# Kernel tuning notes

Measured on AMD Instinct MI355X. Metric: run time of the kernel, lower is better.

Reference implementation:

```python
import jax, jax.numpy as jnp
import numpy as np

N = 50000   # num_entities
F = 300     # node feature dim
D = 128     # embedding_dim
H = 4       # heads
C = D // H  # per-head out channels (32)
E = 640000  # num edges
R = 200     # num_relations
L = 2       # num_layers
NEG_SLOPE = 0.2  # PyG GATv2Conv default


def setup_inputs() -> dict:
    key = jax.random.key(0)
    ks = jax.random.split(key, 14)
    s = 0.1
    return {
        "entity": jnp.arange(N, dtype=jnp.int32),
        "edge_index": jax.random.randint(ks[0], (2, E), 0, N, dtype=jnp.int32),
        "edge_type": jax.random.randint(ks[1], (E,), 0, R, dtype=jnp.int32),
        # learned parameters
        "node_features": jax.random.normal(ks[2], (N, F), jnp.float32) * s,   # entity_embedding table
        "rel_emb": jax.random.normal(ks[3], (R, D), jnp.float32) * s,          # relation_embedding
        "proj_w": jax.random.normal(ks[4], (F, D), jnp.float32) * s,           # project Linear
        "proj_b": jnp.zeros((D,), jnp.float32),
        # per-layer GATv2Conv params, stacked over L layers
        "w_l": jax.random.normal(ks[5], (L, D, H * C), jnp.float32) * s,       # lin_l weight
        "b_l": jnp.zeros((L, H * C), jnp.float32),
        "w_r": jax.random.normal(ks[6], (L, D, H * C), jnp.float32) * s,       # lin_r weight
        "b_r": jnp.zeros((L, H * C), jnp.float32),
        "w_e": jax.random.normal(ks[7], (L, D, H * C), jnp.float32) * s,       # lin_edge weight (no bias)
        "att": jax.random.normal(ks[8], (L, H, C), jnp.float32) * s,           # attention vector a
        "bias": jnp.zeros((L, H * C), jnp.float32),                             # output bias
    }


def _gatv2_layer(x, src, dst, edge_attr, w_l, b_l, w_r, b_r, w_e, att, bias):
    # x: [N, D], edge_attr: [E, D]
    x_l = (x @ w_l + b_l).reshape(N, H, C)
    x_r = (x @ w_r + b_r).reshape(N, H, C)
    e = (edge_attr @ w_e).reshape(E, H, C)
    # per-edge message (gather src/dst + edge), GATv2: leaky_relu BEFORE attention dot
    m = jax.nn.leaky_relu(x_l[src] + x_r[dst] + e, NEG_SLOPE)   # [E, H, C]
    logits = jnp.einsum('ehc,hc->eh', m, att)                    # [E, H]
    # segment softmax over edges grouped by destination node
    lmax = jax.ops.segment_max(logits, dst, num_segments=N)      # [N, H]
    ex = jnp.exp(logits - lmax[dst])                             # [E, H]
    denom = jax.ops.segment_sum(ex, dst, num_segments=N)         # [N, H]
    alpha = ex / denom[dst]                                      # [E, H]
    # scatter-aggregate messages x_l[src] weighted by alpha
    out = jax.ops.segment_sum(x_l[src] * alpha[:, :, None], dst, num_segments=N)  # [N, H, C]
    return out.reshape(N, H * C) + bias


def reference(entity, edge_index, edge_type, node_features, rel_emb,
              proj_w, proj_b, w_l, b_l, w_r, b_r, w_e, att, bias):
    x = node_features[entity]            # embedding lookup
    x = x @ proj_w + proj_b              # project to D
    edge_attr = rel_emb[edge_type]       # [E, D] (weights=False -> no edge_weight scaling)
    src, dst = edge_index[0], edge_index[1]
    for i in range(L):
        x = _gatv2_layer(x, src, dst, edge_attr,
                         w_l[i], b_l[i], w_r[i], b_r[i], w_e[i], att[i], bias[i])
        if i != L - 1:
            x = jax.nn.elu(x)            # dropout inactive (eval mode)
    return x
```

## Files before the change

kernel.cpp:

```cpp
#include <hip/hip_runtime.h>

#define NN 50000
#define FF 300
#define DD 128
#define HH 4
#define CC 32
#define EE 640000
#define RR 200
#define LL 2
#define SB ((NN + 255) / 256)
#define PK 320
#define WCONV (2 * 128 * 128)
#define WTOT (2 * 128 * PK + WCONV)
#define HB2 (EE / 1024)
#define WB2 (WCONV / 1024)
#define FB2 80
#define RB2 100
#define NCH (NN * (PK / 8))
#define CVB3 ((NCH + 1023) / 1024)
#define SCB (EE / 1024)

typedef unsigned short u16;
typedef unsigned int u32;
typedef unsigned long long u64;
typedef _Float16 h2   __attribute__((ext_vector_type(2)));
typedef _Float16 half8 __attribute__((ext_vector_type(8)));
typedef __attribute__((ext_vector_type(4))) float floatx4;
typedef u32 u32x4 __attribute__((ext_vector_type(4)));
typedef u32 u32x2 __attribute__((ext_vector_type(2)));

__device__ __forceinline__ u16 f2h(float f) {
    union { _Float16 h; u16 u; } v; v.h = (_Float16)f; return v.u;
}
__device__ __forceinline__ h2 u2h2(u32 p) {
    union { u32 u; h2 h; } v; v.u = p; return v.h;
}
__device__ __forceinline__ h2 hmax2(h2 a, h2 b) {
#if __has_builtin(__builtin_elementwise_max)
    return __builtin_elementwise_max(a, b);
#else
    h2 r; r.x = a.x > b.x ? a.x : b.x; r.y = a.y > b.y ? a.y : b.y; return r;
#endif
}
__device__ __forceinline__ float hdot2(h2 a, h2 b, float c) {
#if __has_builtin(__builtin_amdgcn_fdot2)
    return __builtin_amdgcn_fdot2(a, b, c, false);
#else
    return c + (float)a.x * (float)b.x + (float)a.y * (float)b.y;
#endif
}
__device__ __forceinline__ void glds16(const void* g, void* l) {
    using gp = const unsigned int __attribute__((address_space(1)))*;
    using lp = unsigned int __attribute__((address_space(3)))*;
    __builtin_amdgcn_global_load_lds((gp)(u64)g, (lp)(u64)l, 16, 0, 0);
}

__device__ __forceinline__ int block_excl_scan(int v, int* lds4, int* total) {
    int lane = threadIdx.x & 63, wid = threadIdx.x >> 6;
    int x = v;
    #pragma unroll
    for (int off = 1; off < 64; off <<= 1) {
        int y = __shfl_up(x, off, 64);
        if (lane >= off) x += y;
    }
    if (lane == 63) lds4[wid] = x;
    __syncthreads();
    int add = 0;
    #pragma unroll
    for (int w = 0; w < 4; w++) add += (w < wid) ? lds4[w] : 0;
    *total = lds4[0] + lds4[1] + lds4[2] + lds4[3];
    return x + add - v;
}

__global__ __launch_bounds__(256)
void prep_kernel(const int* __restrict__ ei, int* __restrict__ counts,
                 const float* __restrict__ proj_w, const float* __restrict__ w_l,
                 const float* __restrict__ w_r, u16* __restrict__ wt,
                 const float* __restrict__ rel_emb, const float* __restrict__ w_e,
                 u16* __restrict__ erel, const float* __restrict__ proj_b,
                 const float* __restrict__ b_l, const float* __restrict__ b_r,
                 float* __restrict__ fbias, const int* __restrict__ entity,
                 const float* __restrict__ nf, u16* __restrict__ xh)
{
    __shared__ float sm[8 * DD];
    int b = blockIdx.x, tid = threadIdx.x;
    if (b < HB2) {
        #pragma unroll
        for (int j = 0; j < 4; j++)
            atomicAdd(&counts[ei[EE + b * 1024 + j * 256 + tid]], 1);
    } else if (b < HB2 + WB2) {
        #pragma unroll
        for (int j = 0; j < 4; j++) {
            int i = (b - HB2) * 1024 + j * 256 + tid;
            int seg = i >> 14;
            int r = i & 16383;
            int n = r >> 7, k = r & 127;
            const float* src = (seg == 0 ? w_l : w_r) + (size_t)DD * DD;
            wt[2 * 128 * PK + i] = f2h(src[(size_t)k * DD + n]);
        }
    } else if (b < HB2 + WB2 + FB2) {
        int bb = b - HB2 - WB2;
        int lr = bb / 40, kg = bb % 40;
        int half = tid >> 7, d = tid & 127;
        int k0 = kg * 8 + half * 4;
        float* rv = sm + half * 4 * DD;
        #pragma unroll
        for (int kk = 0; kk < 4; kk++)
            rv[kk * DD + d] = (k0 + kk < FF) ? proj_w[(size_t)(k0 + kk) * DD + d] : 0.f;
        __syncthreads();
        const float* W = lr ? w_r : w_l;
        float acc[4] = {0.f, 0.f, 0.f, 0.f};
        #pragma unroll 8
        for (int j = 0; j < DD; j++) {
            float wv = W[(size_t)j * DD + d];
            #pragma unroll
            for (int kk = 0; kk < 4; kk++) acc[kk] += rv[kk * DD + j] * wv;
        }
        u16 o[4];
        #pragma unroll
        for (int kk = 0; kk < 4; kk++) o[kk] = f2h(acc[kk]);
        *(u32x2*)(wt + (size_t)lr * 128 * PK + (size_t)d * PK + k0) = *(u32x2*)o;
    } else if (b == HB2 + WB2 + FB2) {
        int half = tid >> 7, d = tid & 127;
        if (tid < DD) sm[tid] = proj_b[tid];
        __syncthreads();
        const float* W = half ? w_r : w_l;
        float acc = half ? b_r[d] : b_l[d];
        #pragma unroll 8
        for (int j = 0; j < DD; j++) acc += sm[j] * W[(size_t)j * DD + d];
        fbias[half * DD + d] = acc;
    } else if (b < HB2 + WB2 + FB2 + 1 + RB2) {
        int bb = b - (HB2 + WB2 + FB2 + 1);
        int l = bb / 50, rg = bb % 50;
        int half = tid >> 7, d = tid & 127;
        int r0 = rg * 4 + half * 2;
        float* rv = sm + half * 2 * DD;
        #pragma unroll
        for (int rr = 0; rr < 2; rr++)
            rv[rr * DD + d] = rel_emb[(size_t)(r0 + rr) * DD + d];
        __syncthreads();
        const float* W = w_e + (size_t)l * DD * DD;
        float acc[2] = {0.f, 0.f};
        #pragma unroll 8
        for (int j = 0; j < DD; j++) {
            float wv = W[(size_t)j * DD + d];
            #pragma unroll
            for (int rr = 0; rr < 2; rr++) acc[rr] += rv[rr * DD + j] * wv;
        }
        #pragma unroll
        for (int rr = 0; rr < 2; rr++)
            erel[(size_t)(l * RR + r0 + rr) * DD + d] = f2h(acc[rr]);
    } else {
        int base = (b - (HB2 + WB2 + FB2 + 1 + RB2)) * 1024 + tid;
        #pragma unroll
        for (int j = 0; j < 4; j++) {
            int ci = base + j * 256;
            if (ci < NCH) {
                int row = ci / (PK / 8);
                int col = (ci - row * (PK / 8)) * 8;
                int xrow = entity[row];
                const float* src = nf + (size_t)xrow * FF + col;
                u16 o[8];
                if (col + 8 <= FF) {
                    float4 f0 = *(const float4*)src;
                    float4 f1 = *(const float4*)(src + 4);
                    o[0] = f2h(f0.x); o[1] = f2h(f0.y); o[2] = f2h(f0.z); o[3] = f2h(f0.w);
                    o[4] = f2h(f1.x); o[5] = f2h(f1.y); o[6] = f2h(f1.z); o[7] = f2h(f1.w);
                } else {
                    #pragma unroll
                    for (int jj = 0; jj < 8; jj++)
                        o[jj] = (col + jj < FF) ? f2h(src[jj]) : (u16)0;
                }
                *(half8*)(xh + (size_t)row * PK + col) = *(half8*)o;
            }
        }
    }
}

template<int K>
__global__ __launch_bounds__(512)
void gemm_gll_kernel(const u16* __restrict__ A,
                     const u16* __restrict__ BT1, const float* __restrict__ bias1,
                     u16* __restrict__ C1,
                     const u16* __restrict__ BT2, const float* __restrict__ bias2,
                     u16* __restrict__ C2, int M)
{
    __shared__ u16 As[64 * 64];
    __shared__ u16 Bs[256 * 64];
    int tid  = threadIdx.x;
    int m0   = blockIdx.x * 64;
    int wave = tid >> 6, lane = tid & 63;
    int quad = lane >> 4, l16 = lane & 15;

    floatx4 acc[4][2];
    #pragma unroll
    for (int i = 0; i < 4; i++)
        #pragma unroll
        for (int j = 0; j < 2; j++) acc[i][j] = (floatx4){0.f, 0.f, 0.f, 0.f};

    int arl = wave * 8 + (lane >> 3);
    int arg = m0 + arl; if (arg >= M) arg = M - 1;
    const char* ap = (const char*)(A + (size_t)arg * K)
                   + (((lane & 7) << 4) ^ ((arl & 7) << 4));
    const char* bp[4];
    #pragma unroll
    for (int c = 0; c < 4; c++) {
        int rowB = wave * 32 + c * 8 + (lane >> 3);
        const u16* base = (rowB < 128) ? BT1 : BT2;
        int br = rowB & 127;
        bp[c] = (const char*)(base + (size_t)br * K)
              + (((lane & 7) << 4) ^ ((br & 7) << 4));
    }
    char* AsW = (char*)As;
    char* BsW = (char*)Bs;
    const char* AsR = (const char*)As;
    const char* BsR = (const char*)Bs;
    int axor = (l16 & 7) << 4;

    for (int kk = 0; kk < K; kk += 64) {
        glds16(ap + kk * 2, AsW + wave * 1024);
        #pragma unroll
        for (int c = 0; c < 4; c++)
            glds16(bp[c] + kk * 2, BsW + (wave * 4 + c) * 1024);
        __syncthreads();
        #pragma unroll
        for (int s2 = 0; s2 < 2; s2++) {
            int cb = (s2 * 64 + quad * 16) ^ axor;
            half8 af[4], bf[2];
            #pragma unroll
            for (int i = 0; i < 4; i++)
                af[i] = *(const half8*)(AsR + (i * 16 + l16) * 128 + cb);
            #pragma unroll
            for (int j = 0; j < 2; j++)
                bf[j] = *(const half8*)(BsR + (wave * 32 + j * 16 + l16) * 128 + cb);
            #pragma unroll
            for (int i = 0; i < 4; i++) {
                acc[i][0] = __builtin_amdgcn_mfma_f32_16x16x32_f16(af[i], bf[0], acc[i][0], 0, 0, 0);
                acc[i][1] = __builtin_amdgcn_mfma_f32_16x16x32_f16(af[i], bf[1], acc[i][1], 0, 0, 0);
            }
        }
        __syncthreads();
    }

    u16* Cw = (wave < 4) ? C1 : C2;
    const float* bw = (wave < 4) ? bias1 : bias2;
    int cb0 = (wave & 3) * 32;
    #pragma unroll
    for (int i = 0; i < 4; i++) {
        #pragma unroll
        for (int rr = 0; rr < 4; rr++) {
            int row = m0 + i * 16 + quad * 4 + rr;
            if (row < M) {
                #pragma unroll
                for (int j = 0; j < 2; j++) {
                    int col = cb0 + j * 16 + l16;
                    Cw[(size_t)row * DD + col] = f2h(acc[i][j][rr] + bw[col]);
                }
            }
        }
    }
}

__global__ __launch_bounds__(256)
void scan_local_kernel(const int* __restrict__ counts, int* __restrict__ offsets,
                       int* __restrict__ bsum)
{
    __shared__ int lds4[4];
    int i = blockIdx.x * 256 + threadIdx.x;
    int v = (i < NN) ? counts[i] : 0;
    int total;
    int ex = block_excl_scan(v, lds4, &total);
    if (i < NN) offsets[i] = ex;
    if (threadIdx.x == 0) bsum[blockIdx.x] = total;
}

__global__ __launch_bounds__(256)
void scan_bsum_kernel(int* __restrict__ bsum)
{
    __shared__ int lds4[4];
    int t = threadIdx.x;
    int v = (t < SB) ? bsum[t] : 0;
    int total;
    int ex = block_excl_scan(v, lds4, &total);
    if (t < SB) bsum[t] = ex;
}

__global__ __launch_bounds__(256)
void scatter_kernel(const int* __restrict__ ei, const int* __restrict__ et,
                    const int* __restrict__ offsets, const int* __restrict__ bsum,
                    int* __restrict__ fill, u32* __restrict__ dstorder)
{
    #pragma unroll
    for (int j = 0; j < 4; j++) {
        int e = blockIdx.x * 1024 + j * 256 + threadIdx.x;
        int d = ei[EE + e];
        int pos = offsets[d] + bsum[d >> 8] + atomicAdd(&fill[d], 1);
        dstorder[pos] = (u32)ei[e] | ((u32)et[e] << 16);
    }
}

__global__ __launch_bounds__(256)
void node_kernel(const u32* __restrict__ dstorder, const int* __restrict__ offsets,
                 const int* __restrict__ bsum,
                 const u16* __restrict__ xl, const u16* __restrict__ xr,
                 const u16* __restrict__ erel, const float* __restrict__ att,
                 const float* __restrict__ bias,
                 u16* __restrict__ xnext, float* __restrict__ outp, int is_last)
{
    int tid  = threadIdx.x;
    int node = blockIdx.x * 4 + (tid >> 6);
    int lane = tid & 63;
    if (node >= NN) return;
    int g  = lane >> 4;
    int gl = lane & 15;
    int c0 = gl * 8;
    int beg = offsets[node] + bsum[node >> 8];
    int end = (node == NN - 1) ? EE : offsets[node + 1] + bsum[(node + 1) >> 8];

    h2 xrh[4], atth[4];
    {
        u32x4 xrv = *(const u32x4*)(xr + ((u32)node * DD + c0));
        #pragma unroll
        for (int q = 0; q < 4; q++) xrh[q] = u2h2(xrv[q]);
        #pragma unroll
        for (int q = 0; q < 4; q++) {
            float2 av = *(const float2*)&att[c0 + q * 2];
            atth[q] = (h2){(_Float16)av.x, (_Float16)av.y};
        }
    }
    const h2 c02 = (h2){(_Float16)0.2f, (_Float16)0.2f};

    float s = 0.f;
    h2 a2[4];
    #pragma unroll
    for (int q = 0; q < 4; q++) a2[q] = (h2){(_Float16)0.f, (_Float16)0.f};

    for (int base = beg; base < end; base += 4) {
        int es = base + g;
        bool valid = es < end;
        u32 st = valid ? dstorder[es] : 0;
        u32 xoff = (st & 0xffffu) * DD + (u32)c0;
        u32 eoff = (st >> 16) * DD + (u32)c0;
        u32x4 xv = *(const u32x4*)(xl + xoff);
        u32x4 ev = *(const u32x4*)(erel + eoff);
        h2 xh[4];
        float p = 0.f;
        #pragma unroll
        for (int q = 0; q < 4; q++) {
            xh[q] = u2h2(xv[q]);
            h2 m = (xh[q] + xrh[q]) + u2h2(ev[q]);
            m = hmax2(m, m * c02);
            p = hdot2(m, atth[q], p);
        }
        p += __shfl_xor(p, 1, 64);
        p += __shfl_xor(p, 2, 64);
        float w = valid ? __expf(fminf(p, 60.f)) : 0.f;
        s += w;
        h2 wh = (h2){(_Float16)w, (_Float16)w};
        #pragma unroll
        for (int q = 0; q < 4; q++) a2[q] += wh * xh[q];
    }

    float a[8];
    #pragma unroll
    for (int q = 0; q < 4; q++) { a[q*2] = (float)a2[q].x; a[q*2+1] = (float)a2[q].y; }
    #pragma unroll
    for (int j = 0; j < 8; j++) {
        a[j] += __shfl_xor(a[j], 16, 64);
        a[j] += __shfl_xor(a[j], 32, 64);
    }
    s += __shfl_xor(s, 16, 64);
    s += __shfl_xor(s, 32, 64);

    if (lane < 16) {
        float rh = 1.f / fmaxf(s, 1e-30f);
        float4 b0 = *(const float4*)&bias[c0];
        float4 b1 = *(const float4*)&bias[c0 + 4];
        float bv[8] = {b0.x, b0.y, b0.z, b0.w, b1.x, b1.y, b1.z, b1.w};
        float v[8];
        #pragma unroll
        for (int j = 0; j < 8; j++) v[j] = a[j] * rh + bv[j];
        if (is_last) {
            float4* op = (float4*)(outp + ((u32)node * DD + c0));
            op[0] = make_float4(v[0], v[1], v[2], v[3]);
            op[1] = make_float4(v[4], v[5], v[6], v[7]);
        } else {
            u16 pk[8];
            #pragma unroll
            for (int j = 0; j < 8; j++) {
                float w2 = v[j] > 0.f ? v[j] : __expf(v[j]) - 1.f;
                pk[j] = f2h(w2);
            }
            *(half8*)(xnext + ((u32)node * DD + c0)) = *(half8*)pk;
        }
    }
}

extern "C" void kernel_launch(void* const* d_in, const int* in_sizes, int n_in,
                              void* d_out, int out_size, void* d_ws, size_t ws_size,
                              hipStream_t stream)
{
    const int*   entity        = (const int*)d_in[0];
    const int*   edge_index    = (const int*)d_in[1];
    const int*   edge_type     = (const int*)d_in[2];
    const float* node_features = (const float*)d_in[3];
    const float* rel_emb       = (const float*)d_in[4];
    const float* proj_w        = (const float*)d_in[5];
    const float* proj_b        = (const float*)d_in[6];
    const float* w_l           = (const float*)d_in[7];
    const float* b_l           = (const float*)d_in[8];
    const float* w_r           = (const float*)d_in[9];
    const float* b_r           = (const float*)d_in[10];
    const float* w_e           = (const float*)d_in[11];
    const float* att           = (const float*)d_in[12];
    const float* bias          = (const float*)d_in[13];

    u16*   xb      = (u16*)d_ws;
    u16*   xl      = xb + (size_t)NN * DD;
    u16*   xr      = xl + (size_t)NN * DD;
    u16*   erel    = xr + (size_t)NN * DD;
    u16*   wt      = erel + (size_t)LL * RR * DD;
    u32*   dstorder= (u32*)(wt + WTOT);
    int*   counts  = (int*)(dstorder + (size_t)EE);
    int*   fill    = counts + NN;
    int*   offsets = fill + NN;
    int*   bsum    = offsets + NN;
    float* fbias   = (float*)(bsum + SB);
    u16*   xh      = (u16*)(fbias + 2 * DD);

    hipMemsetAsync(counts, 0, (size_t)NN * 2 * sizeof(int), stream);
    prep_kernel<<<HB2 + WB2 + FB2 + 1 + RB2 + CVB3, 256, 0, stream>>>(
        edge_index, counts, proj_w, w_l, w_r, wt, rel_emb, w_e, erel,
        proj_b, b_l, b_r, fbias, entity, node_features, xh);

    scan_local_kernel<<<SB, 256, 0, stream>>>(counts, offsets, bsum);
    scan_bsum_kernel<<<1, 256, 0, stream>>>(bsum);
    scatter_kernel<<<SCB, 256, 0, stream>>>(
        edge_index, edge_type, offsets, bsum, fill, dstorder);

    const int GB2 = (NN + 63) / 64;

    gemm_gll_kernel<PK><<<GB2, 512, 0, stream>>>(
        xh, wt, fbias, xl,
        wt + (size_t)128 * PK, fbias + DD, xr, NN);
    node_kernel<<<(NN + 3) / 4, 256, 0, stream>>>(
        dstorder, offsets, bsum, xl, xr, erel,
        att, bias, xb, (float*)d_out, 0);

    gemm_gll_kernel<DD><<<GB2, 512, 0, stream>>>(
        xb, wt + (size_t)2 * 128 * PK, b_l + DD, xl,
        wt + (size_t)2 * 128 * PK + 128 * 128, b_r + DD, xr, NN);
    node_kernel<<<(NN + 3) / 4, 256, 0, stream>>>(
        dstorder, offsets, bsum, xl, xr, erel + (size_t)RR * DD,
        att + DD, bias + DD, xb, (float*)d_out, 1);
}
```

Before: 335.6 us.

## Fuse entity gather and fp32-to-fp16 conversion into first-layer GEMM A-load

Drops the separate prep stage that gathered node_features rows by entity, converted them to fp16 and padded them into a staging buffer. The first GEMM now loads fp32 rows straight from node_features through the entity index into LDS, converts to fp16 while building MFMA fragments, and handles the 44-column tail with a guarded scalar load. This removes one write and one read of a 50000x320 fp16 intermediate. In exchange it doubles LDS for the A tile, reads fp32 (twice the bytes) inside the GEMM, and adds conversion work to the inner loop.

```diff
diff --git a/kernel.cpp b/kernel.cpp
--- a/kernel.cpp
+++ b/kernel.cpp
@@ -16,8 +16,7 @@
 #define WB2 (WCONV / 1024)
 #define FB2 80
 #define RB2 100
-#define NCH (NN * (PK / 8))
-#define CVB3 ((NCH + 1023) / 1024)
+#define PB (HB2 + WB2 + FB2 + 1 + RB2)
 #define SCB (EE / 1024)
 
 typedef unsigned short u16;
@@ -79,8 +78,7 @@
                  const float* __restrict__ rel_emb, const float* __restrict__ w_e,
                  u16* __restrict__ erel, const float* __restrict__ proj_b,
                  const float* __restrict__ b_l, const float* __restrict__ b_r,
-                 float* __restrict__ fbias, const int* __restrict__ entity,
-                 const float* __restrict__ nf, u16* __restrict__ xh)
+                 float* __restrict__ fbias)
 {
     __shared__ float sm[8 * DD];
     int b = blockIdx.x, tid = threadIdx.x;
@@ -129,7 +127,7 @@
         #pragma unroll 8
         for (int j = 0; j < DD; j++) acc += sm[j] * W[(size_t)j * DD + d];
         fbias[half * DD + d] = acc;
-    } else if (b < HB2 + WB2 + FB2 + 1 + RB2) {
+    } else {
         int bb = b - (HB2 + WB2 + FB2 + 1);
         int l = bb / 50, rg = bb % 50;
         int half = tid >> 7, d = tid & 127;
@@ -150,42 +148,18 @@
         #pragma unroll
         for (int rr = 0; rr < 2; rr++)
             erel[(size_t)(l * RR + r0 + rr) * DD + d] = f2h(acc[rr]);
-    } else {
-        int base = (b - (HB2 + WB2 + FB2 + 1 + RB2)) * 1024 + tid;
-        #pragma unroll
-        for (int j = 0; j < 4; j++) {
-            int ci = base + j * 256;
-            if (ci < NCH) {
-                int row = ci / (PK / 8);
-                int col = (ci - row * (PK / 8)) * 8;
-                int xrow = entity[row];
-                const float* src = nf + (size_t)xrow * FF + col;
-                u16 o[8];
-                if (col + 8 <= FF) {
-                    float4 f0 = *(const float4*)src;
-                    float4 f1 = *(const float4*)(src + 4);
-                    o[0] = f2h(f0.x); o[1] = f2h(f0.y); o[2] = f2h(f0.z); o[3] = f2h(f0.w);
-                    o[4] = f2h(f1.x); o[5] = f2h(f1.y); o[6] = f2h(f1.z); o[7] = f2h(f1.w);
-                } else {
-                    #pragma unroll
-                    for (int jj = 0; jj < 8; jj++)
-                        o[jj] = (col + jj < FF) ? f2h(src[jj]) : (u16)0;
-                }
-                *(half8*)(xh + (size_t)row * PK + col) = *(half8*)o;
-            }
-        }
-    }
-}
-
-template<int K>
+    }
+}
+
+template<int K, bool AF32>
 __global__ __launch_bounds__(512)
-void gemm_gll_kernel(const u16* __restrict__ A,
+void gemm_gll_kernel(const void* __restrict__ A_, const int* __restrict__ rowidx,
                      const u16* __restrict__ BT1, const float* __restrict__ bias1,
                      u16* __restrict__ C1,
                      const u16* __restrict__ BT2, const float* __restrict__ bias2,
                      u16* __restrict__ C2, int M)
 {
-    __shared__ u16 As[64 * 64];
+    __shared__ float AsF[AF32 ? 4096 : 2048];
     __shared__ u16 Bs[256 * 64];
     int tid  = threadIdx.x;
     int m0   = blockIdx.x * 64;
@@ -198,10 +172,6 @@
         #pragma unroll
         for (int j = 0; j < 2; j++) acc[i][j] = (floatx4){0.f, 0.f, 0.f, 0.f};
 
-    int arl = wave * 8 + (lane >> 3);
-    int arg = m0 + arl; if (arg >= M) arg = M - 1;
-    const char* ap = (const char*)(A + (size_t)arg * K)
-                   + (((lane & 7) << 4) ^ ((arl & 7) << 4));
     const char* bp[4];
     #pragma unroll
     for (int c = 0; c < 4; c++) {
@@ -211,35 +181,107 @@
         bp[c] = (const char*)(base + (size_t)br * K)
               + (((lane & 7) << 4) ^ ((br & 7) << 4));
     }
-    char* AsW = (char*)As;
+    char* AsW = (char*)AsF;
     char* BsW = (char*)Bs;
-    const char* AsR = (const char*)As;
+    const char* AsR = (const char*)AsF;
     const char* BsR = (const char*)Bs;
-    int axor = (l16 & 7) << 4;
-
-    for (int kk = 0; kk < K; kk += 64) {
-        glds16(ap + kk * 2, AsW + wave * 1024);
-        #pragma unroll
-        for (int c = 0; c < 4; c++)
-            glds16(bp[c] + kk * 2, BsW + (wave * 4 + c) * 1024);
-        __syncthreads();
-        #pragma unroll
-        for (int s2 = 0; s2 < 2; s2++) {
-            int cb = (s2 * 64 + quad * 16) ^ axor;
+
+    const char* ap1; const char* ap2; const float* s1; const float* s2;
+    int r1, r2;
+    if constexpr (AF32) {
+        r1 = wave * 4 + (lane >> 4);
+        r2 = r1 + 32;
+        int g1 = m0 + r1; if (g1 >= M) g1 = M - 1;
+        int g2 = m0 + r2; if (g2 >= M) g2 = M - 1;
+        s1 = (const float*)A_ + (size_t)rowidx[g1] * FF;
+        s2 = (const float*)A_ + (size_t)rowidx[g2] * FF;
+        ap1 = (const char*)s1 + (((lane & 15) ^ (r1 & 7)) * 16);
+        ap2 = (const char*)s2 + (((lane & 15) ^ (r2 & 7)) * 16);
+    } else {
+        int arl = wave * 8 + (lane >> 3);
+        int arg = m0 + arl; if (arg >= M) arg = M - 1;
+        ap1 = (const char*)((const u16*)A_ + (size_t)arg * K)
+            + (((lane & 7) << 4) ^ ((arl & 7) << 4));
+        ap2 = nullptr; s1 = s2 = nullptr; r1 = r2 = 0;
+    }
+    int axor16 = (l16 & 7) << 4;
+
+    auto compute = [&]() {
+        #pragma unroll
+        for (int s2i = 0; s2i < 2; s2i++) {
             half8 af[4], bf[2];
-            #pragma unroll
-            for (int i = 0; i < 4; i++)
-                af[i] = *(const half8*)(AsR + (i * 16 + l16) * 128 + cb);
+            if constexpr (AF32) {
+                int c0 = s2i * 8 + quad * 2;
+                #pragma unroll
+                for (int i = 0; i < 4; i++) {
+                    int row = i * 16 + l16;
+                    const char* rb = AsR + row * 256;
+                    float4 lo = *(const float4*)(rb + ((c0 ^ (row & 7)) * 16));
+                    float4 hi = *(const float4*)(rb + (((c0 + 1) ^ (row & 7)) * 16));
+                    u16 o[8];
+                    o[0] = f2h(lo.x); o[1] = f2h(lo.y); o[2] = f2h(lo.z); o[3] = f2h(lo.w);
+                    o[4] = f2h(hi.x); o[5] = f2h(hi.y); o[6] = f2h(hi.z); o[7] = f2h(hi.w);
+                    af[i] = *(half8*)o;
+                }
+            } else {
+                int cb = (s2i * 64 + quad * 16) ^ axor16;
+                #pragma unroll
+                for (int i = 0; i < 4; i++)
+                    af[i] = *(const half8*)(AsR + (i * 16 + l16) * 128 + cb);
+            }
+            int cbB = (s2i * 64 + quad * 16) ^ axor16;
             #pragma unroll
             for (int j = 0; j < 2; j++)
-                bf[j] = *(const half8*)(BsR + (wave * 32 + j * 16 + l16) * 128 + cb);
+                bf[j] = *(const half8*)(BsR + (wave * 32 + j * 16 + l16) * 128 + cbB);
             #pragma unroll
             for (int i = 0; i < 4; i++) {
                 acc[i][0] = __builtin_amdgcn_mfma_f32_16x16x32_f16(af[i], bf[0], acc[i][0], 0, 0, 0);
                 acc[i][1] = __builtin_amdgcn_mfma_f32_16x16x32_f16(af[i], bf[1], acc[i][1], 0, 0, 0);
             }
         }
+    };
+
+    if constexpr (AF32) {
+        #pragma unroll
+        for (int kk = 0; kk < 256; kk += 64) {
+            glds16(ap1 + kk * 4, AsW + wave * 1024);
+            glds16(ap2 + kk * 4, AsW + 8192 + wave * 1024);
+            #pragma unroll
+            for (int c = 0; c < 4; c++)
+                glds16(bp[c] + kk * 2, BsW + (wave * 4 + c) * 1024);
+            __syncthreads();
+            compute();
+            __syncthreads();
+        }
+        #pragma unroll
+        for (int c = 0; c < 4; c++)
+            glds16(bp[c] + 256 * 2, BsW + (wave * 4 + c) * 1024);
+        {
+            int gc1 = (lane & 15) ^ (r1 & 7);
+            int gc2 = (lane & 15) ^ (r2 & 7);
+            float v1[4] = {0, 0, 0, 0}, v2[4] = {0, 0, 0, 0};
+            #pragma unroll
+            for (int j = 0; j < 4; j++) {
+                int col1 = 256 + gc1 * 4 + j;
+                int col2 = 256 + gc2 * 4 + j;
+                if (col1 < FF) v1[j] = s1[col1];
+                if (col2 < FF) v2[j] = s2[col2];
+            }
+            *(float4*)(AsW + r1 * 256 + (lane & 15) * 16) = make_float4(v1[0], v1[1], v1[2], v1[3]);
+            *(float4*)(AsW + r2 * 256 + (lane & 15) * 16) = make_float4(v2[0], v2[1], v2[2], v2[3]);
+        }
         __syncthreads();
+        compute();
+    } else {
+        for (int kk = 0; kk < K; kk += 64) {
+            glds16(ap1 + kk * 2, AsW + wave * 1024);
+            #pragma unroll
+            for (int c = 0; c < 4; c++)
+                glds16(bp[c] + kk * 2, BsW + (wave * 4 + c) * 1024);
+            __syncthreads();
+            compute();
+            __syncthreads();
+        }
     }
 
     u16* Cw = (wave < 4) ? C1 : C2;
@@ -426,12 +468,11 @@
     int*   offsets = fill + NN;
     int*   bsum    = offsets + NN;
     float* fbias   = (float*)(bsum + SB);
-    u16*   xh      = (u16*)(fbias + 2 * DD);
 
     hipMemsetAsync(counts, 0, (size_t)NN * 2 * sizeof(int), stream);
-    prep_kernel<<<HB2 + WB2 + FB2 + 1 + RB2 + CVB3, 256, 0, stream>>>(
+    prep_kernel<<<PB, 256, 0, stream>>>(
         edge_index, counts, proj_w, w_l, w_r, wt, rel_emb, w_e, erel,
-        proj_b, b_l, b_r, fbias, entity, node_features, xh);
+        proj_b, b_l, b_r, fbias);
 
     scan_local_kernel<<<SB, 256, 0, stream>>>(counts, offsets, bsum);
     scan_bsum_kernel<<<1, 256, 0, stream>>>(bsum);
@@ -440,15 +481,15 @@
 
     const int GB2 = (NN + 63) / 64;
 
-    gemm_gll_kernel<PK><<<GB2, 512, 0, stream>>>(
-        xh, wt, fbias, xl,
+    gemm_gll_kernel<PK, true><<<GB2, 512, 0, stream>>>(
+        node_features, entity, wt, fbias, xl,
         wt + (size_t)128 * PK, fbias + DD, xr, NN);
     node_kernel<<<(NN + 3) / 4, 256, 0, stream>>>(
         dstorder, offsets, bsum, xl, xr, erel,
         att, bias, xb, (float*)d_out, 0);
 
-    gemm_gll_kernel<DD><<<GB2, 512, 0, stream>>>(
-        xb, wt + (size_t)2 * 128 * PK, b_l + DD, xl,
+    gemm_gll_kernel<DD, false><<<GB2, 512, 0, stream>>>(
+        xb, nullptr, wt + (size_t)2 * 128 * PK, b_l + DD, xl,
         wt + (size_t)2 * 128 * PK + 128 * 128, b_r + DD, xr, NN);
     node_kernel<<<(NN + 3) / 4, 256, 0, stream>>>(
         dstorder, offsets, bsum, xl, xr, erel + (size_t)RR * DD,
```

Result: faster. 316.4 us (-5.7%).
